# Performance work log

Hardware: AMD Instinct MI355X
Metric: run time of the kernel (lower is better)

Reference implementation:

```python
import jax, jax.numpy as jnp
import numpy as np

B, IN_UNITS, IN_CHANNELS, NUM_UNITS, UNIT_SIZE = 128, 32, 4096, 10, 16
NUM_ITER = 3


def setup_inputs() -> dict:
    key = jax.random.key(0)
    k1, k2 = jax.random.split(key)
    # x: primary-capsule output [B, in_units, in_channels]
    x = jax.random.normal(k1, (B, IN_UNITS, IN_CHANNELS), dtype=jnp.float32)
    # W: routing weights, torch param shape [1, C, J, D, K] with batch dim dropped
    W = jax.random.normal(k2, (IN_CHANNELS, NUM_UNITS, UNIT_SIZE, IN_UNITS), dtype=jnp.float32)
    return {"x": x, "W": W}


def reference(x, W):
    b_sz = x.shape[0]
    C, J = W.shape[0], W.shape[1]
    # torch: x.transpose(1,2) -> [B,C,K]; u_hat = W @ x -> [B,C,J,D,1]
    # u_hat[b,i,j,d] = sum_k W[i,j,d,k] * x[b,k,i]
    u_hat = jnp.einsum('ijdk,bki->bijd', W, x)  # [B, C, J, D]
    b_ij = jnp.zeros((C, J), dtype=x.dtype)
    v = None
    for _ in range(NUM_ITER):
        # faithful: softmax over dim=1 (in_channels axis), not over classes
        c_ij = jax.nn.softmax(b_ij, axis=0)               # [C, J]
        s = jnp.einsum('ij,bijd->bjd', c_ij, u_hat)        # [B, J, D]
        # faithful squash: original sums over dim=2 of [B,1,J,D,1] == class axis J
        mag_sq = jnp.sum(s * s, axis=1, keepdims=True)     # [B, 1, D]
        v = (mag_sq / (1.0 + mag_sq)) * (s / jnp.sqrt(mag_sq))
        # agreement: <u_hat, v> averaged over batch
        agree = jnp.einsum('bijd,bjd->ij', u_hat, v) / b_sz
        b_ij = b_ij + agree
    # torch returns v_j.squeeze(1): [B, J, D, 1]
    return v[:, :, :, None]
```

## Files before the change

### kernel.cpp

```cpp
#include <hip/hip_runtime.h>


typedef __attribute__((ext_vector_type(8))) __bf16 bf16x8;
typedef __attribute__((ext_vector_type(4))) float  f32x4;
typedef __attribute__((ext_vector_type(8))) unsigned short u16x8;
typedef __attribute__((ext_vector_type(4))) unsigned int  u32x4;

#define DI __device__ __forceinline__

DI float bf2f(unsigned short u){ unsigned int x = ((unsigned int)u) << 16; return __builtin_bit_cast(float, x); }
DI unsigned short f2bf(float f){
  unsigned int u = __builtin_bit_cast(unsigned int, f);
  u += 0x7fffu + ((u >> 16) & 1u);
  return (unsigned short)(u >> 16);
}
DI unsigned int cvtpk(float lo, float hi){
  unsigned int r;
  asm("v_cvt_pk_bf16_f32 %0, %1, %2" : "=v"(r) : "v"(lo), "v"(hi));
  return r;
}

constexpr int Ci = 4096, Kk = 32, Jj = 10, Dd = 16, Bb = 128;
constexpr int KI = Ci * Kk;
constexpr int JDt = Jj * Dd;
constexpr int NCH = 256, CK = 512;

constexpr size_t OFF_XB = 0;
constexpr size_t SZ_XB  = (size_t)Bb * KI * 2;
constexpr size_t OFF_W2 = OFF_XB + SZ_XB;
constexpr size_t SZ_W2  = (size_t)JDt * KI * 2;
constexpr size_t OFF_BT = OFF_W2 + SZ_W2;
constexpr size_t SZ_BT  = (size_t)Jj * Ci * 4;
constexpr size_t OFF_CT = OFF_BT + SZ_BT;
constexpr size_t OFF_VBT = OFF_CT + SZ_BT;
constexpr size_t SZ_VBT = (size_t)JDt * Bb * 2;
constexpr size_t OFF_SP = OFF_VBT + SZ_VBT;
constexpr size_t SZ_SP  = (size_t)NCH * Bb * JDt * 4;

constexpr int WPAD = 522;
__global__ __launch_bounds__(512) void pack_w(const float* __restrict__ W, unsigned short* __restrict__ w2){
  __shared__ unsigned short t16[64 * WPAD];
  const int mt = blockIdx.x % 10, it = blockIdx.x / 10;
  const int m0 = mt * 512, i0 = it * 64;
  #pragma unroll
  for(int u=0; u<16; u++){
    int e = threadIdx.x + 512*u;
    int row = e >> 7, c4 = e & 127;
    float4 v = *(const float4*)(W + (size_t)(i0+row)*5120 + m0 + c4*4);
    unsigned int* p = (unsigned int*)(t16 + row*WPAD + c4*4);
    p[0] = cvtpk(v.x, v.y);
    p[1] = cvtpk(v.z, v.w);
  }
  __syncthreads();
  #pragma unroll
  for(int u=0; u<8; u++){
    int e = threadIdx.x + 512*u;
    int mr = e >> 3, g = e & 7;
    u32x4 o;
    #pragma unroll
    for(int j=0; j<4; j++){
      unsigned int lo = t16[(g*8 + 2*j    )*WPAD + mr];
      unsigned int hi = t16[(g*8 + 2*j + 1)*WPAD + mr];
      o[j] = lo | (hi << 16);
    }
    *(u32x4*)(w2 + (size_t)(m0+mr)*Ci + i0 + g*8) = o;
  }
}

__global__ __launch_bounds__(256) void pack_x(const float* __restrict__ x, unsigned short* __restrict__ xbf,
                                              float* __restrict__ bT){
  const int bid = blockIdx.x;
  if(bid >= 8192){
    ((f32x4*)bT)[(bid-8192)*256 + threadIdx.x] = f32x4{0.f,0.f,0.f,0.f};
    return;
  }
  const size_t e = (size_t)bid * 256 + threadIdx.x;
  const float4* xv = (const float4*)x;
  float4 a = xv[e*2], b = xv[e*2+1];
  u32x4 o;
  o[0]=cvtpk(a.x,a.y); o[1]=cvtpk(a.z,a.w);
  o[2]=cvtpk(b.x,b.y); o[3]=cvtpk(b.z,b.w);
  *(u32x4*)(xbf + e*8) = o;
}

__global__ __launch_bounds__(256) void softmax_k(const float* __restrict__ bT, float* __restrict__ cT){
  const int j = blockIdx.x, tid = threadIdx.x, lane = tid & 63, wid = tid >> 6;
  __shared__ float red[4];
  float vals[16];
  float mx = -3.4e38f;
  #pragma unroll
  for(int u=0; u<16; u++){ vals[u] = bT[j*Ci + tid + 256*u]; mx = fmaxf(mx, vals[u]); }
  #pragma unroll
  for(int o=32; o>0; o>>=1) mx = fmaxf(mx, __shfl_xor(mx, o));
  if(lane == 0) red[wid] = mx;
  __syncthreads();
  mx = fmaxf(fmaxf(red[0],red[1]), fmaxf(red[2],red[3]));
  float sm = 0.f;
  #pragma unroll
  for(int u=0; u<16; u++){ vals[u] = expf(vals[u]-mx); sm += vals[u]; }
  #pragma unroll
  for(int o=32; o>0; o>>=1) sm += __shfl_xor(sm, o);
  __syncthreads();
  if(lane == 0) red[wid] = sm;
  __syncthreads();
  sm = red[0]+red[1]+red[2]+red[3];
  float inv = 1.0f / sm;
  #pragma unroll
  for(int u=0; u<16; u++) cT[j*Ci + tid + 256*u] = vals[u]*inv;
}

__global__ __launch_bounds__(512) void s_pass(const unsigned short* __restrict__ xb,
                                              const unsigned short* __restrict__ w2,
                                              const float* __restrict__ cT,
                                              float* __restrict__ spart){
  __shared__ unsigned short xs[128*64];
  __shared__ unsigned short wsm[160*64];
  const int tid = threadIdx.x, lane = tid & 63, wid = tid >> 6;
  const int wb = wid & 3, wj = wid >> 2;
  const int ki0 = blockIdx.x * CK;
  f32x4 acc[2][5];
  const f32x4 z = {0.f,0.f,0.f,0.f};
  #pragma unroll
  for(int m=0;m<2;m++){ acc[m][0]=z; acc[m][1]=z; acc[m][2]=z; acc[m][3]=z; acc[m][4]=z; }

  for(int step=0; step<CK/64; ++step){
    const int kb = ki0 + step*64;
    const int ib = kb & (Ci-1);
    #pragma unroll
    for(int u=0; u<2; u++){
      int e = tid + 512*u;
      int b = e >> 3, sg = e & 7;
      u16x8 v = *(const u16x8*)(xb + (size_t)b*KI + kb + sg*8);
      *(u16x8*)((char*)xs + b*128 + ((sg*16) ^ ((b&7)<<4))) = v;
    }
    #pragma unroll
    for(int u=0; u<3; u++){
      int e = tid + 512*u;
      if(e < 1280){
        int jd = e >> 3, sg = e & 7;
        u16x8 v = *(const u16x8*)(w2 + (size_t)jd*KI + kb + sg*8);
        float cc[8];
        if(cT){
          const float* cp = cT + (jd>>4)*Ci + ib + sg*8;
          float4 c0 = *(const float4*)cp;
          float4 c1 = *(const float4*)(cp+4);
          cc[0]=c0.x; cc[1]=c0.y; cc[2]=c0.z; cc[3]=c0.w;
          cc[4]=c1.x; cc[5]=c1.y; cc[6]=c1.z; cc[7]=c1.w;
        } else {
          #pragma unroll
          for(int q=0;q<8;q++) cc[q] = (1.0f/4096.0f);
        }
        u16x8 o;
        #pragma unroll
        for(int q=0;q<8;q++) o[q] = f2bf(bf2f(v[q])*cc[q]);
        *(u16x8*)((char*)wsm + jd*128 + ((sg*16) ^ ((jd&7)<<4))) = o;
      }
    }
    __syncthreads();
    #pragma unroll
    for(int ks=0; ks<2; ks++){
      const int kk2 = (ks*32 + ((lane>>4)<<3)) * 2;
      bf16x8 a[2];
      #pragma unroll
      for(int m=0;m<2;m++){
        int row = wb*32 + m*16 + (lane&15);
        a[m] = *(const bf16x8*)((const char*)xs + row*128 + (kk2 ^ ((row&7)<<4)));
      }
      #pragma unroll
      for(int n=0;n<5;n++){
        int row = wj*80 + n*16 + (lane&15);
        bf16x8 bb = *(const bf16x8*)((const char*)wsm + row*128 + (kk2 ^ ((row&7)<<4)));
        acc[0][n] = __builtin_amdgcn_mfma_f32_16x16x32_bf16(a[0], bb, acc[0][n], 0,0,0);
        acc[1][n] = __builtin_amdgcn_mfma_f32_16x16x32_bf16(a[1], bb, acc[1][n], 0,0,0);
      }
    }
    __syncthreads();
  }
  float* sp = spart + (size_t)blockIdx.x * (Bb*JDt);
  #pragma unroll
  for(int m=0;m<2;m++)
    #pragma unroll
    for(int n=0;n<5;n++)
      #pragma unroll
      for(int r=0;r<4;r++){
        int b  = wb*32 + m*16 + ((lane>>4)<<2) + r;
        int jd = wj*80 + n*16 + (lane&15);
        sp[b*JDt + jd] = acc[m][n][r];
      }
}

__global__ __launch_bounds__(256) void redsq(const float* __restrict__ spart,
                                             float* __restrict__ vout,
                                             unsigned short* __restrict__ vbT){
  const int b = blockIdx.x, tid = threadIdx.x;
  __shared__ float sq[JDt];
  __shared__ float scale[Dd];
  float s = 0.f;
  if(tid < JDt){
    const float* p = spart + b*JDt + tid;
    #pragma unroll 8
    for(int ch=0; ch<NCH; ch++) s += p[(size_t)ch*(Bb*JDt)];
    sq[tid] = s*s;
  }
  __syncthreads();
  if(tid < Dd){
    float m = 0.f;
    #pragma unroll
    for(int j=0;j<Jj;j++) m += sq[j*Dd + tid];
    scale[tid] = sqrtf(m) / (1.0f + m);
  }
  __syncthreads();
  if(tid < JDt){
    float v = s * scale[tid & (Dd-1)];
    vout[b*JDt + tid] = v;
    vbT[tid*Bb + b] = f2bf(v);
  }
}

__global__ __launch_bounds__(256) void agree_pass(const unsigned short* __restrict__ xb,
                                                  const unsigned short* __restrict__ vbT,
                                                  const unsigned short* __restrict__ w2,
                                                  float* __restrict__ bT){
  __shared__ unsigned short xsT[64*128];
  __shared__ unsigned short vsm[160*128];
  const int tid = threadIdx.x, lane = tid & 63, wid = tid >> 6;
  const int wj = wid & 1, wk = wid >> 1;
  const int ki0 = blockIdx.x * 64;
  #pragma unroll
  for(int u=0; u<4; u++){
    int e = tid + 256*u;
    int b = e >> 3, sg = e & 7;
    u16x8 v = *(const u16x8*)(xb + (size_t)b*KI + ki0 + sg*8);
    #pragma unroll
    for(int q=0; q<8; q++){
      int kil = sg*8 + q;
      *(unsigned short*)((char*)xsT + kil*256 + ((b*2) ^ ((kil&7)<<4))) = v[q];
    }
  }
  #pragma unroll
  for(int u=0; u<10; u++){
    int e = tid + 256*u;
    int jd = e >> 4, sg = e & 15;
    u16x8 v = *(const u16x8*)(vbT + jd*Bb + sg*8);
    *(u16x8*)((char*)vsm + jd*256 + ((sg*16) ^ ((jd&7)<<4))) = v;
  }
  __syncthreads();
  f32x4 acc[5][2];
  const f32x4 z = {0.f,0.f,0.f,0.f};
  #pragma unroll
  for(int m=0;m<5;m++){ acc[m][0]=z; acc[m][1]=z; }
  #pragma unroll
  for(int ks=0; ks<4; ks++){
    const int b2 = (ks*32 + ((lane>>4)<<3)) * 2;
    bf16x8 bfr[2];
    #pragma unroll
    for(int n=0;n<2;n++){
      int row = wk*32 + n*16 + (lane&15);
      bfr[n] = *(const bf16x8*)((const char*)xsT + row*256 + (b2 ^ ((row&7)<<4)));
    }
    #pragma unroll
    for(int m=0;m<5;m++){
      int row = wj*80 + m*16 + (lane&15);
      bf16x8 af = *(const bf16x8*)((const char*)vsm + row*256 + (b2 ^ ((row&7)<<4)));
      acc[m][0] = __builtin_amdgcn_mfma_f32_16x16x32_bf16(af, bfr[0], acc[m][0], 0,0,0);
      acc[m][1] = __builtin_amdgcn_mfma_f32_16x16x32_bf16(af, bfr[1], acc[m][1], 0,0,0);
    }
  }
  const int ibase = ki0 & (Ci-1);
  #pragma unroll
  for(int m=0;m<5;m++){
    int j = wj*5 + m;
    #pragma unroll
    for(int n=0;n<2;n++){
      int colg = ki0 + wk*32 + n*16 + (lane&15);
      float s = 0.f;
      #pragma unroll
      for(int r=0;r<4;r++){
        int jdrow = wj*80 + m*16 + ((lane>>4)<<2) + r;
        s += acc[m][n][r] * bf2f(w2[(size_t)jdrow*KI + colg]);
      }
      s += __shfl_xor(s, 16);
      s += __shfl_xor(s, 32);
      if(lane < 16){
        int ig = ibase + wk*32 + n*16 + lane;
        atomicAdd(bT + j*Ci + ig, s * (1.0f/128.0f));
      }
    }
  }
}

extern "C" void kernel_launch(void* const* d_in, const int* in_sizes, int n_in,
                              void* d_out, int out_size, void* d_ws, size_t ws_size,
                              hipStream_t stream) {
  const float* x = (const float*)d_in[0];
  const float* W = (const float*)d_in[1];
  float* out = (float*)d_out;
  char* ws = (char*)d_ws;
  unsigned short* xbf = (unsigned short*)(ws + OFF_XB);
  unsigned short* w2  = (unsigned short*)(ws + OFF_W2);
  float* bT           = (float*)(ws + OFF_BT);
  float* cT           = (float*)(ws + OFF_CT);
  unsigned short* vbT = (unsigned short*)(ws + OFF_VBT);
  float* spart        = (float*)(ws + OFF_SP);

  pack_w<<<640, 512, 0, stream>>>(W, w2);
  pack_x<<<8232, 256, 0, stream>>>(x, xbf, bT);
  for(int t=0; t<3; t++){
    if(t > 0) softmax_k<<<Jj, 256, 0, stream>>>(bT, cT);
    s_pass<<<NCH, 512, 0, stream>>>(xbf, w2, (t==0)? nullptr : cT, spart);
    redsq<<<Bb, 256, 0, stream>>>(spart, out, vbT);
    if(t < 2) agree_pass<<<KI/64, 256, 0, stream>>>(xbf, vbT, w2, bT);
  }
}
```

Before: 229.7 us.

## Fuse softmax into s_pass and merge pack kernels into one launch

Removes the separate softmax kernel. Each s_pass block now computes the per-class max and sum of bT with an online softmax, then applies exp and normalisation inline when scaling the W tile. The pack_w and pack_x kernels are also merged into one pack_all launch that covers W packing, x conversion and zeroing of bT. This saves three launches and the cT round trip, at the cost of every one of the 256 blocks redundantly reading all 40K bT entries and doing extra exp work.

After: 234.8 us. +2.2%, slower.

```diff
diff --git a/kernel.cpp b/kernel.cpp
--- a/kernel.cpp
+++ b/kernel.cpp
@@ -31,93 +31,93 @@
 constexpr size_t SZ_W2  = (size_t)JDt * KI * 2;
 constexpr size_t OFF_BT = OFF_W2 + SZ_W2;
 constexpr size_t SZ_BT  = (size_t)Jj * Ci * 4;
-constexpr size_t OFF_CT = OFF_BT + SZ_BT;
-constexpr size_t OFF_VBT = OFF_CT + SZ_BT;
+constexpr size_t OFF_VBT = OFF_BT + SZ_BT;
 constexpr size_t SZ_VBT = (size_t)JDt * Bb * 2;
 constexpr size_t OFF_SP = OFF_VBT + SZ_VBT;
 constexpr size_t SZ_SP  = (size_t)NCH * Bb * JDt * 4;
 
 constexpr int WPAD = 522;
-__global__ __launch_bounds__(512) void pack_w(const float* __restrict__ W, unsigned short* __restrict__ w2){
+__global__ __launch_bounds__(512) void pack_all(const float* __restrict__ x, const float* __restrict__ W,
+                                                unsigned short* __restrict__ xbf, unsigned short* __restrict__ w2,
+                                                float* __restrict__ bT){
   __shared__ unsigned short t16[64 * WPAD];
-  const int mt = blockIdx.x % 10, it = blockIdx.x / 10;
-  const int m0 = mt * 512, i0 = it * 64;
-  #pragma unroll
-  for(int u=0; u<16; u++){
-    int e = threadIdx.x + 512*u;
-    int row = e >> 7, c4 = e & 127;
-    float4 v = *(const float4*)(W + (size_t)(i0+row)*5120 + m0 + c4*4);
-    unsigned int* p = (unsigned int*)(t16 + row*WPAD + c4*4);
-    p[0] = cvtpk(v.x, v.y);
-    p[1] = cvtpk(v.z, v.w);
-  }
-  __syncthreads();
-  #pragma unroll
-  for(int u=0; u<8; u++){
-    int e = threadIdx.x + 512*u;
-    int mr = e >> 3, g = e & 7;
+  const int bid = blockIdx.x;
+  if(bid < 640){
+    const int mt = bid % 10, it = bid / 10;
+    const int m0 = mt * 512, i0 = it * 64;
+    #pragma unroll
+    for(int u=0; u<16; u++){
+      int e = threadIdx.x + 512*u;
+      int row = e >> 7, c4 = e & 127;
+      float4 v = *(const float4*)(W + (size_t)(i0+row)*5120 + m0 + c4*4);
+      unsigned int* p = (unsigned int*)(t16 + row*WPAD + c4*4);
+      p[0] = cvtpk(v.x, v.y);
+      p[1] = cvtpk(v.z, v.w);
+    }
+    __syncthreads();
+    #pragma unroll
+    for(int u=0; u<8; u++){
+      int e = threadIdx.x + 512*u;
+      int mr = e >> 3, g = e & 7;
+      u32x4 o;
+      #pragma unroll
+      for(int j=0; j<4; j++){
+        unsigned int lo = t16[(g*8 + 2*j    )*WPAD + mr];
+        unsigned int hi = t16[(g*8 + 2*j + 1)*WPAD + mr];
+        o[j] = lo | (hi << 16);
+      }
+      *(u32x4*)(w2 + (size_t)(m0+mr)*Ci + i0 + g*8) = o;
+    }
+  } else if(bid < 4736){
+    const size_t e = (size_t)(bid - 640) * 512 + threadIdx.x;
+    const float4* xv = (const float4*)x;
+    float4 a = xv[e*2], b = xv[e*2+1];
     u32x4 o;
-    #pragma unroll
-    for(int j=0; j<4; j++){
-      unsigned int lo = t16[(g*8 + 2*j    )*WPAD + mr];
-      unsigned int hi = t16[(g*8 + 2*j + 1)*WPAD + mr];
-      o[j] = lo | (hi << 16);
-    }
-    *(u32x4*)(w2 + (size_t)(m0+mr)*Ci + i0 + g*8) = o;
-  }
-}
-
-__global__ __launch_bounds__(256) void pack_x(const float* __restrict__ x, unsigned short* __restrict__ xbf,
-                                              float* __restrict__ bT){
-  const int bid = blockIdx.x;
-  if(bid >= 8192){
-    ((f32x4*)bT)[(bid-8192)*256 + threadIdx.x] = f32x4{0.f,0.f,0.f,0.f};
-    return;
-  }
-  const size_t e = (size_t)bid * 256 + threadIdx.x;
-  const float4* xv = (const float4*)x;
-  float4 a = xv[e*2], b = xv[e*2+1];
-  u32x4 o;
-  o[0]=cvtpk(a.x,a.y); o[1]=cvtpk(a.z,a.w);
-  o[2]=cvtpk(b.x,b.y); o[3]=cvtpk(b.z,b.w);
-  *(u32x4*)(xbf + e*8) = o;
-}
-
-__global__ __launch_bounds__(256) void softmax_k(const float* __restrict__ bT, float* __restrict__ cT){
-  const int j = blockIdx.x, tid = threadIdx.x, lane = tid & 63, wid = tid >> 6;
-  __shared__ float red[4];
-  float vals[16];
-  float mx = -3.4e38f;
-  #pragma unroll
-  for(int u=0; u<16; u++){ vals[u] = bT[j*Ci + tid + 256*u]; mx = fmaxf(mx, vals[u]); }
-  #pragma unroll
-  for(int o=32; o>0; o>>=1) mx = fmaxf(mx, __shfl_xor(mx, o));
-  if(lane == 0) red[wid] = mx;
-  __syncthreads();
-  mx = fmaxf(fmaxf(red[0],red[1]), fmaxf(red[2],red[3]));
-  float sm = 0.f;
-  #pragma unroll
-  for(int u=0; u<16; u++){ vals[u] = expf(vals[u]-mx); sm += vals[u]; }
-  #pragma unroll
-  for(int o=32; o>0; o>>=1) sm += __shfl_xor(sm, o);
-  __syncthreads();
-  if(lane == 0) red[wid] = sm;
-  __syncthreads();
-  sm = red[0]+red[1]+red[2]+red[3];
-  float inv = 1.0f / sm;
-  #pragma unroll
-  for(int u=0; u<16; u++) cT[j*Ci + tid + 256*u] = vals[u]*inv;
+    o[0]=cvtpk(a.x,a.y); o[1]=cvtpk(a.z,a.w);
+    o[2]=cvtpk(b.x,b.y); o[3]=cvtpk(b.z,b.w);
+    *(u32x4*)(xbf + e*8) = o;
+  } else {
+    ((f32x4*)bT)[(size_t)(bid-4736)*512 + threadIdx.x] = f32x4{0.f,0.f,0.f,0.f};
+  }
 }
 
 __global__ __launch_bounds__(512) void s_pass(const unsigned short* __restrict__ xb,
                                               const unsigned short* __restrict__ w2,
-                                              const float* __restrict__ cT,
+                                              const float* __restrict__ bT,
                                               float* __restrict__ spart){
   __shared__ unsigned short xs[128*64];
   __shared__ unsigned short wsm[160*64];
+  __shared__ float jmx[Jj], jinv[Jj];
   const int tid = threadIdx.x, lane = tid & 63, wid = tid >> 6;
   const int wb = wid & 3, wj = wid >> 2;
   const int ki0 = blockIdx.x * CK;
+
+  if(bT){
+    for(int j = wid; j < Jj; j += 8){
+      float m = -3.4e38f, s = 0.f;
+      const float* row = bT + j*Ci;
+      #pragma unroll
+      for(int c0 = 0; c0 < 8; ++c0){
+        const float* p = row + lane*8 + c0*512;
+        f32x4 a = *(const f32x4*)p;
+        f32x4 b = *(const f32x4*)(p+4);
+        #pragma unroll
+        for(int q=0;q<4;q++){ float v=a[q]; float m2=fmaxf(m,v); s = s*__expf(m-m2)+__expf(v-m2); m=m2; }
+        #pragma unroll
+        for(int q=0;q<4;q++){ float v=b[q]; float m2=fmaxf(m,v); s = s*__expf(m-m2)+__expf(v-m2); m=m2; }
+      }
+      #pragma unroll
+      for(int o=32;o>0;o>>=1){
+        float mo = __shfl_xor(m,o), so = __shfl_xor(s,o);
+        float m2 = fmaxf(m, mo);
+        s = s*__expf(m-m2) + so*__expf(mo-m2);
+        m = m2;
+      }
+      if(lane==0){ jmx[j] = m; jinv[j] = 1.0f / s; }
+    }
+  }
+  __syncthreads();
+
   f32x4 acc[2][5];
   const f32x4 z = {0.f,0.f,0.f,0.f};
   #pragma unroll
@@ -140,12 +140,16 @@
         int jd = e >> 3, sg = e & 7;
         u16x8 v = *(const u16x8*)(w2 + (size_t)jd*KI + kb + sg*8);
         float cc[8];
-        if(cT){
-          const float* cp = cT + (jd>>4)*Ci + ib + sg*8;
-          float4 c0 = *(const float4*)cp;
-          float4 c1 = *(const float4*)(cp+4);
-          cc[0]=c0.x; cc[1]=c0.y; cc[2]=c0.z; cc[3]=c0.w;
-          cc[4]=c1.x; cc[5]=c1.y; cc[6]=c1.z; cc[7]=c1.w;
+        if(bT){
+          const int j = jd >> 4;
+          const float* bp = bT + j*Ci + ib + sg*8;
+          f32x4 b0 = *(const f32x4*)bp;
+          f32x4 b1 = *(const f32x4*)(bp+4);
+          const float mxj = jmx[j], ivj = jinv[j];
+          cc[0]=__expf(b0[0]-mxj)*ivj; cc[1]=__expf(b0[1]-mxj)*ivj;
+          cc[2]=__expf(b0[2]-mxj)*ivj; cc[3]=__expf(b0[3]-mxj)*ivj;
+          cc[4]=__expf(b1[0]-mxj)*ivj; cc[5]=__expf(b1[1]-mxj)*ivj;
+          cc[6]=__expf(b1[2]-mxj)*ivj; cc[7]=__expf(b1[3]-mxj)*ivj;
         } else {
           #pragma unroll
           for(int q=0;q<8;q++) cc[q] = (1.0f/4096.0f);
@@ -299,15 +303,12 @@
   unsigned short* xbf = (unsigned short*)(ws + OFF_XB);
   unsigned short* w2  = (unsigned short*)(ws + OFF_W2);
   float* bT           = (float*)(ws + OFF_BT);
-  float* cT           = (float*)(ws + OFF_CT);
   unsigned short* vbT = (unsigned short*)(ws + OFF_VBT);
   float* spart        = (float*)(ws + OFF_SP);
 
-  pack_w<<<640, 512, 0, stream>>>(W, w2);
-  pack_x<<<8232, 256, 0, stream>>>(x, xbf, bT);
+  pack_all<<<4756, 512, 0, stream>>>(x, W, xbf, w2, bT);
   for(int t=0; t<3; t++){
-    if(t > 0) softmax_k<<<Jj, 256, 0, stream>>>(bT, cT);
-    s_pass<<<NCH, 512, 0, stream>>>(xbf, w2, (t==0)? nullptr : cT, spart);
+    s_pass<<<NCH, 512, 0, stream>>>(xbf, w2, (t==0)? nullptr : bT, spart);
     redsq<<<Bb, 256, 0, stream>>>(spart, out, vbT);
     if(t < 2) agree_pass<<<KI/64, 256, 0, stream>>>(xbf, vbT, w2, bT);
   }
```
